# Optimization experiments

Measured on AMD Instinct MI355X. Metric: run time of the kernel, lower is better.

## Reference

```python
import jax, jax.numpy as jnp
import numpy as np

N, T, V = 32, 4096, 3
H = 512
CONNECTIVITY = 0.3
SPECTRAL_RADIUS = 0.99
NOISE_LEVEL = 0.01
N_DROP = 0


def _init_internal_weights(h, connectivity, spectral_radius):
    # Mirrors sparse.rand(...).todense(); nonzeros shifted by -0.5; normalized
    # so max |eigenvalue| == spectral_radius.
    rng = np.random.default_rng(0)
    w = rng.random((h, h)).astype(np.float32)
    mask = rng.random((h, h)) < connectivity
    w = np.where(mask, w - 0.5, 0.0).astype(np.float32)
    e_max = np.abs(np.linalg.eigvals(w)).max()
    w = w / (e_max / spectral_radius)
    return jnp.asarray(w, dtype=jnp.float32)


def setup_inputs() -> dict:
    key = jax.random.key(0)
    k_x, k_in, k_noise = jax.random.split(key, 3)
    X = jax.random.normal(k_x, (N, T, V), dtype=jnp.float32)
    # input weights: (2*bernoulli(U(0,1)) - 1) * 0.2  -> random signs * 0.2
    signs = 2.0 * jax.random.bernoulli(k_in, 0.5, (H, V)).astype(jnp.float32) - 1.0
    W_in = signs * 0.2
    W_int = _init_internal_weights(H, CONNECTIVITY, SPECTRAL_RADIUS)
    # per-step uniform noise, pre-drawn: (T, N, H)
    noise = jax.random.uniform(k_noise, (T, N, H), dtype=jnp.float32)
    return {"X": X, "W_in": W_in, "W_int": W_int, "noise": noise}


def reference(X, W_in, W_int, noise):
    # X: (N, T, V); W_in: (H, V); W_int: (H, H); noise: (T, N, H)
    n, t, _ = X.shape
    h = W_int.shape[0]
    # einsum('bij,kj->bki', X, W_in) indexed [:, :, t] == per-step input (N, H)
    inputs = jnp.einsum('btv,hv->tbh', X, W_in)  # (T, N, H)
    prev0 = jnp.full((n, h), 0.01, dtype=X.dtype)

    def step(prev, xs):
        x_t, n_t = xs
        s = jnp.tanh(prev @ W_int + x_t + n_t * NOISE_LEVEL)
        return s, s

    _, states = jax.lax.scan(step, prev0, (inputs, noise))  # (T, N, H)
    states = jnp.transpose(states, (1, 0, 2))  # (N, T, H)
    return states[:, N_DROP:, :]
```

## Files before the change

kernel.cpp:

```cpp
#include <hip/hip_runtime.h>
#include <stdint.h>

typedef _Float16 h2 __attribute__((ext_vector_type(2)));
typedef float    f4 __attribute__((ext_vector_type(4)));

#if __has_builtin(__builtin_amdgcn_fdot2)
__device__ __forceinline__ float dot2(uint32_t a, uint32_t b, float c) {
    return __builtin_amdgcn_fdot2(__builtin_bit_cast(h2, a),
                                  __builtin_bit_cast(h2, b), c, false);
}
#else
__device__ __forceinline__ float dot2(uint32_t a, uint32_t b, float c) {
    h2 ha = __builtin_bit_cast(h2, a), hb = __builtin_bit_cast(h2, b);
    return c + (float)ha[0]*(float)hb[0] + (float)ha[1]*(float)hb[1];
}
#endif

#define TT 4096
#define NB 32
#define HD 512
#define JL 16
#define JTOT 64
#define JR (JTOT - JL)
#define WSTRIDE 65

__global__ __launch_bounds__(512, 2)
void esn_kernel(const float* __restrict__ X, const float* __restrict__ W_in,
                const float* __restrict__ W_int, const float* __restrict__ noise,
                float* __restrict__ out)
{
    __shared__ _Float16 s_buf[2][HD];
    __shared__ float    pads[4][HD];
    __shared__ uint32_t wstash[512 * WSTRIDE];

    const int tid  = threadIdx.x;
    const int b    = blockIdx.x;
    const int kg   = tid >> 7;
    const int colg = tid & 127;
    const int c0   = colg * 4;

    const float win0 = W_in[tid*3 + 0];
    const float win1 = W_in[tid*3 + 1];
    const float win2 = W_in[tid*3 + 2];

    uint32_t wreg[4][JR];
    {
        const f4* Wv = (const f4*)W_int;
        for (int j = 0; j < JL; ++j) {
            const int k = kg*128 + 2*j;
            f4 r0 = Wv[(size_t)k*128 + colg];
            f4 r1 = Wv[(size_t)(k+1)*128 + colg];
            #pragma unroll
            for (int c = 0; c < 4; ++c) {
                h2 w; w[0] = (_Float16)r0[c]; w[1] = (_Float16)r1[c];
                wstash[tid*WSTRIDE + j*4 + c] = __builtin_bit_cast(uint32_t, w);
            }
        }
        #pragma unroll
        for (int j = 0; j < JR; ++j) {
            const int k = kg*128 + 2*(JL + j);
            f4 r0 = Wv[(size_t)k*128 + colg];
            f4 r1 = Wv[(size_t)(k+1)*128 + colg];
            #pragma unroll
            for (int c = 0; c < 4; ++c) {
                h2 w; w[0] = (_Float16)r0[c]; w[1] = (_Float16)r1[c];
                wreg[c][j] = __builtin_bit_cast(uint32_t, w);
            }
        }
    }
    s_buf[0][tid] = (_Float16)0.01f;
    __syncthreads();

    const float* Xb   = X   + (size_t)b * TT * 3;
    float*       outb = out + (size_t)b * TT * HD;
    const size_t nb   = (size_t)b * HD + tid;

    int cur = 0;
    for (int t = 0; t < TT; ++t) {
        const float nz = noise[(size_t)t*(NB*HD) + nb];
        const float x0 = Xb[t*3 + 0];
        const float x1 = Xb[t*3 + 1];
        const float x2 = Xb[t*3 + 2];

        const uint32_t* s32 = (const uint32_t*)(&s_buf[cur][0]);
        const int sb = kg*64;
        float a0 = 0.f, a1 = 0.f, a2 = 0.f, a3 = 0.f;

        #pragma unroll
        for (int j = 0; j < JL; ++j) {
            const uint32_t sv = s32[sb + j];
            const int wb = tid*WSTRIDE + j*4;
            a0 = dot2(sv, wstash[wb+0], a0);
            a1 = dot2(sv, wstash[wb+1], a1);
            a2 = dot2(sv, wstash[wb+2], a2);
            a3 = dot2(sv, wstash[wb+3], a3);
        }
        #pragma unroll
        for (int j = 0; j < JR; ++j) {
            const uint32_t sv = s32[sb + JL + j];
            a0 = dot2(sv, wreg[0][j], a0);
            a1 = dot2(sv, wreg[1][j], a1);
            a2 = dot2(sv, wreg[2][j], a2);
            a3 = dot2(sv, wreg[3][j], a3);
        }
        f4 pv; pv[0] = a0; pv[1] = a1; pv[2] = a2; pv[3] = a3;
        *(f4*)&pads[kg][c0] = pv;
        __syncthreads();

        float z = pads[0][tid] + pads[1][tid] + pads[2][tid] + pads[3][tid];
        z += win0*x0 + win1*x1 + win2*x2 + 0.01f*nz;
        const float s = tanhf(z);
        outb[(size_t)t*HD + tid] = s;
        s_buf[cur^1][tid] = (_Float16)s;
        __syncthreads();
        cur ^= 1;
    }
}

extern "C" void kernel_launch(void* const* d_in, const int* in_sizes, int n_in,
                              void* d_out, int out_size, void* d_ws, size_t ws_size,
                              hipStream_t stream)
{
    const float* X     = (const float*)d_in[0];
    const float* W_in  = (const float*)d_in[1];
    const float* W_int = (const float*)d_in[2];
    const float* noise = (const float*)d_in[3];
    float* out = (float*)d_out;

    esn_kernel<<<dim3(NB), dim3(512), 0, stream>>>(X, W_in, W_int, noise, out);
}
```

Baseline: 6.619 ms.

## Vectorize LDS weight/state reads, shift more weights to registers, fast tanh

Lays out the LDS weight stash as lane-contiguous 128-bit vectors per wave so each step does one wide conflict-free load instead of four strided scalar loads. The hidden state is also read from LDS as 128-bit vectors. More weight pairs move from LDS to registers (JL 16 to 12), and the occupancy hint changes to waves_per_eu(2,2). tanhf is replaced with an exp/rcp approximation to shorten the serial per-step tail. The cost is more register pressure, a possible spill, and slightly lower tanh accuracy, including overflow handling of exp for large inputs.

```diff
diff --git a/kernel.cpp b/kernel.cpp
--- a/kernel.cpp
+++ b/kernel.cpp
@@ -3,6 +3,7 @@
 
 typedef _Float16 h2 __attribute__((ext_vector_type(2)));
 typedef float    f4 __attribute__((ext_vector_type(4)));
+typedef uint32_t u4 __attribute__((ext_vector_type(4)));
 
 #if __has_builtin(__builtin_amdgcn_fdot2)
 __device__ __forceinline__ float dot2(uint32_t a, uint32_t b, float c) {
@@ -16,25 +17,31 @@
 }
 #endif
 
+__device__ __forceinline__ float fast_tanh(float z) {
+    float e = __expf(2.0f * z);
+    return 1.0f - 2.0f * __builtin_amdgcn_rcpf(e + 1.0f);
+}
+
 #define TT 4096
 #define NB 32
 #define HD 512
-#define JL 16
+#define JL 12
 #define JTOT 64
 #define JR (JTOT - JL)
-#define WSTRIDE 65
 
-__global__ __launch_bounds__(512, 2)
+__global__ __attribute__((amdgpu_waves_per_eu(2, 2))) __launch_bounds__(512)
 void esn_kernel(const float* __restrict__ X, const float* __restrict__ W_in,
                 const float* __restrict__ W_int, const float* __restrict__ noise,
                 float* __restrict__ out)
 {
-    __shared__ _Float16 s_buf[2][HD];
-    __shared__ float    pads[4][HD];
-    __shared__ uint32_t wstash[512 * WSTRIDE];
+    __shared__ __align__(16) _Float16 s_buf[2][HD];
+    __shared__ float pads[4][HD];
+    __shared__ u4 wstash[8 * JL * 64];
 
     const int tid  = threadIdx.x;
     const int b    = blockIdx.x;
+    const int w    = tid >> 6;
+    const int l    = tid & 63;
     const int kg   = tid >> 7;
     const int colg = tid & 127;
     const int c0   = colg * 4;
@@ -50,11 +57,13 @@
             const int k = kg*128 + 2*j;
             f4 r0 = Wv[(size_t)k*128 + colg];
             f4 r1 = Wv[(size_t)(k+1)*128 + colg];
+            u4 q;
             #pragma unroll
             for (int c = 0; c < 4; ++c) {
-                h2 w; w[0] = (_Float16)r0[c]; w[1] = (_Float16)r1[c];
-                wstash[tid*WSTRIDE + j*4 + c] = __builtin_bit_cast(uint32_t, w);
+                h2 hw; hw[0] = (_Float16)r0[c]; hw[1] = (_Float16)r1[c];
+                q[c] = __builtin_bit_cast(uint32_t, hw);
             }
+            wstash[(w*JL + j)*64 + l] = q;
         }
         #pragma unroll
         for (int j = 0; j < JR; ++j) {
@@ -63,8 +72,8 @@
             f4 r1 = Wv[(size_t)(k+1)*128 + colg];
             #pragma unroll
             for (int c = 0; c < 4; ++c) {
-                h2 w; w[0] = (_Float16)r0[c]; w[1] = (_Float16)r1[c];
-                wreg[c][j] = __builtin_bit_cast(uint32_t, w);
+                h2 hw; hw[0] = (_Float16)r0[c]; hw[1] = (_Float16)r1[c];
+                wreg[c][j] = __builtin_bit_cast(uint32_t, hw);
             }
         }
     }
@@ -82,22 +91,25 @@
         const float x1 = Xb[t*3 + 1];
         const float x2 = Xb[t*3 + 2];
 
-        const uint32_t* s32 = (const uint32_t*)(&s_buf[cur][0]);
-        const int sb = kg*64;
+        const u4* sv4 = (const u4*)((const uint32_t*)(&s_buf[cur][0]) + kg*64);
         float a0 = 0.f, a1 = 0.f, a2 = 0.f, a3 = 0.f;
+        u4 sq;
 
         #pragma unroll
         for (int j = 0; j < JL; ++j) {
-            const uint32_t sv = s32[sb + j];
-            const int wb = tid*WSTRIDE + j*4;
-            a0 = dot2(sv, wstash[wb+0], a0);
-            a1 = dot2(sv, wstash[wb+1], a1);
-            a2 = dot2(sv, wstash[wb+2], a2);
-            a3 = dot2(sv, wstash[wb+3], a3);
+            if ((j & 3) == 0) sq = sv4[j >> 2];
+            const uint32_t sv = sq[j & 3];
+            u4 q = wstash[(w*JL + j)*64 + l];
+            a0 = dot2(sv, q[0], a0);
+            a1 = dot2(sv, q[1], a1);
+            a2 = dot2(sv, q[2], a2);
+            a3 = dot2(sv, q[3], a3);
         }
         #pragma unroll
         for (int j = 0; j < JR; ++j) {
-            const uint32_t sv = s32[sb + JL + j];
+            const int jg = JL + j;
+            if ((jg & 3) == 0) sq = sv4[jg >> 2];
+            const uint32_t sv = sq[jg & 3];
             a0 = dot2(sv, wreg[0][j], a0);
             a1 = dot2(sv, wreg[1][j], a1);
             a2 = dot2(sv, wreg[2][j], a2);
@@ -109,7 +121,7 @@
 
         float z = pads[0][tid] + pads[1][tid] + pads[2][tid] + pads[3][tid];
         z += win0*x0 + win1*x1 + win2*x2 + 0.01f*nz;
-        const float s = tanhf(z);
+        const float s = fast_tanh(z);
         outb[(size_t)t*HD + tid] = s;
         s_buf[cur^1][tid] = (_Float16)s;
         __syncthreads();
```

After: 5.375 ms. -18.8%, faster.
